# Optimization experiments

Measured on AMD Instinct MI355X. Metric: run time of the kernel, lower is better.

Reference implementation:

```python
import jax, jax.numpy as jnp
import numpy as np

# ---- FNET: small stride-4 CNN feature extractor (3 -> 64 channels) ----

def _conv(x, w, b, stride, pad):
    y = jax.lax.conv_general_dilated(x, w, (stride, stride), [(pad, pad), (pad, pad)],
                                     dimension_numbers=('NCHW', 'OIHW', 'NCHW'))
    return y + b[None, :, None, None]


def _fnet(x, w1, b1, w2, b2, w3, b3):
    x = jax.nn.relu(_conv(x, w1, b1, 2, 3))   # /2
    x = jax.nn.relu(_conv(x, w2, b2, 2, 1))   # /4
    return _conv(x, w3, b3, 1, 1)             # [N, 64, H/4, W/4]


def _bilinear(feat, u, v):
    # feat: [C, Hf, Wf]; u, v: [D, H, W] pixel coords. Zero padding outside.
    C, Hf, Wf = feat.shape
    u0 = jnp.floor(u); v0 = jnp.floor(v)
    du = u - u0; dv = v - v0
    def gather(ui, vi):
        inb = (ui >= 0) & (ui < Wf) & (vi >= 0) & (vi < Hf)
        uic = jnp.clip(ui, 0, Wf - 1).astype(jnp.int32)
        vic = jnp.clip(vi, 0, Hf - 1).astype(jnp.int32)
        return feat[:, vic, uic] * inb[None].astype(feat.dtype)  # [C, D, H, W]
    f00 = gather(u0, v0);     f01 = gather(u0 + 1, v0)
    f10 = gather(u0, v0 + 1); f11 = gather(u0 + 1, v0 + 1)
    return (f00 * ((1 - du) * (1 - dv))[None] + f01 * (du * (1 - dv))[None]
            + f10 * ((1 - du) * dv)[None] + f11 * (du * dv)[None])


def _magnet_f(ref_img, nghbr_imgs, nghbr_poses, is_valid, cam_intrins, d_center,
              w1, b1, w2, b2, w3, b3):
    B = ref_img.shape[0]
    feat_4 = _fnet(jnp.concatenate([ref_img, nghbr_imgs], axis=0), w1, b1, w2, b2, w3, b3)
    ref_feat = feat_4[:B]                      # [B, C, H4, W4]
    ngh_feat = feat_4[B:]                      # [B*V, C, H4, W4]
    BV = ngh_feat.shape[0]; V = BV // B
    C, H4, W4 = ref_feat.shape[1:]
    D = d_center.shape[1]

    R = nghbr_poses[:, :, :3, :3]              # [B, V, 3, 3]
    t = nghbr_poses[:, :, :3, 3]               # [B, V, 3]
    Kinv = jnp.linalg.inv(cam_intrins)         # [B, 3, 3]

    dt = d_center.dtype
    ys, xs = jnp.meshgrid(jnp.arange(H4, dtype=dt), jnp.arange(W4, dtype=dt), indexing='ij')
    pix = jnp.stack([xs, ys, jnp.ones_like(xs)], 0)          # [3, H4, W4]
    rays = jnp.einsum('bij,jhw->bihw', Kinv, pix)            # [B, 3, H4, W4]
    P = d_center[:, None] * rays[:, :, None]                 # [B, 3, D, H4, W4]
    P_src = jnp.einsum('bvij,bjdhw->bvidhw', R, P) + t[..., None, None, None]
    p = jnp.einsum('bij,bvjdhw->bvidhw', cam_intrins, P_src) # [B, V, 3, D, H4, W4]

    z = p[:, :, 2]
    z_ok = z > 1e-3
    zc = jnp.maximum(z, 1e-3)
    u = p[:, :, 0] / zc
    v = p[:, :, 1] / zc                                      # [B, V, D, H4, W4]
    inb = (u >= 0) & (u <= W4 - 1) & (v >= 0) & (v <= H4 - 1)

    warped = jax.vmap(_bilinear)(ngh_feat,
                                 u.reshape(BV, D, H4, W4),
                                 v.reshape(BV, D, H4, W4))   # [B*V, C, D, H4, W4]
    warped = warped.reshape(B, V, C, D, H4, W4)

    cost = jnp.einsum('bchw,bvcdhw->bvdhw', ref_feat, warped) / C  # [B, V, D, H4, W4]
    mask = (is_valid[:, :, None, None, None] & z_ok & inb).astype(cost.dtype)
    cost_volume = (cost * mask).sum(1) / jnp.maximum(mask.sum(1), 1.0)  # [B, D, H4, W4]
    return cost_volume


def setup_inputs() -> dict:
    B, V, H, W, D, C = 2, 4, 480, 640, 5, 64
    H4, W4 = H // 4, W // 4
    ks = jax.random.split(jax.random.key(0), 12)
    ref_img = jax.random.normal(ks[0], (B, 3, H, W), jnp.float32)
    nghbr_imgs = jax.random.normal(ks[1], (B * V, 3, H, W), jnp.float32)
    # near-identity relative poses with small random translations
    poses = jnp.tile(jnp.eye(4, dtype=jnp.float32), (B, V, 1, 1))
    poses = poses.at[:, :, :3, 3].set(0.05 * jax.random.normal(ks[2], (B, V, 3), jnp.float32))
    is_valid = jnp.ones((B, V), dtype=bool)
    K = jnp.array([[144.0, 0.0, 80.0], [0.0, 144.0, 60.0], [0.0, 0.0, 1.0]], jnp.float32)
    cam_intrins = jnp.tile(K, (B, 1, 1))
    d_center = jax.random.uniform(ks[3], (B, D, H4, W4), jnp.float32, 0.5, 5.0)
    w1 = 0.1 * jax.random.normal(ks[4], (32, 3, 7, 7), jnp.float32); b1 = jnp.zeros((32,), jnp.float32)
    w2 = 0.1 * jax.random.normal(ks[5], (C, 32, 3, 3), jnp.float32); b2 = jnp.zeros((C,), jnp.float32)
    w3 = 0.1 * jax.random.normal(ks[6], (C, C, 3, 3), jnp.float32); b3 = jnp.zeros((C,), jnp.float32)
    return {"ref_img": ref_img, "nghbr_imgs": nghbr_imgs, "nghbr_poses": poses,
            "is_valid": is_valid, "cam_intrins": cam_intrins, "d_center": d_center,
            "w1": w1, "b1": b1, "w2": w2, "b2": b2, "w3": w3, "b3": b3}


def reference(ref_img, nghbr_imgs, nghbr_poses, is_valid, cam_intrins, d_center,
              w1, b1, w2, b2, w3, b3):
    return _magnet_f(ref_img, nghbr_imgs, nghbr_poses, is_valid, cam_intrins, d_center,
                     w1, b1, w2, b2, w3, b3)
```

## Files before the change

kernel.cpp:

```cpp
#include <hip/hip_runtime.h>
#include <hip/hip_bf16.h>

#define B_  2
#define V_  4
#define Hin 480
#define Win 640
#define H2  240
#define W2  320
#define H4  120
#define W4  160
#define C1  32
#define C_  64
#define D_  5
#define NIMG 10

#define P1H 242
#define P1W 322
#define P2H 122
#define P2W 162
#define PIH 486
#define PIW 646

typedef __attribute__((ext_vector_type(8))) short short8;
typedef __attribute__((ext_vector_type(4))) float f32x4;

#define OFF_F1HI 0
#define OFF_F1LO 12467840
#define OFF_F2HI 24935680
#define OFF_F2LO 31260160
#define OFF_INHI 24935680
#define OFF_INLO 29645504
#define OFF_F3   0
#define OFF_GEOM 37584640
#define OFF_W1P  37584736
#define OFF_W2P  37590880
#define OFF_W3P  37609312

__global__ void packw_kernel(const float* __restrict__ w, ushort* __restrict__ dst,
                             int CI, int NK, int lo_off) {
    int idx = blockIdx.x * 256 + threadIdx.x;
    int total = 4 * NK * 64 * 8;
    if (idx >= total) return;
    int j = idx & 7;
    int lane = (idx >> 3) & 63;
    int s = (idx >> 9) % NK;
    int t = idx / (NK * 512);
    int k = s * 32 + (lane >> 4) * 8 + j;
    int co = t * 16 + (lane & 15);
    int kyx = k / CI;
    int ci  = k % CI;
    int ky = kyx / 3, kx = kyx % 3;
    float val = w[((co * CI + ci) * 3 + ky) * 3 + kx];
    __hip_bfloat16 h = __float2bfloat16(val);
    float hf = __bfloat162float(h);
    __hip_bfloat16 l = __float2bfloat16(val - hf);
    dst[idx]          = *reinterpret_cast<ushort*>(&h);
    dst[lo_off + idx] = *reinterpret_cast<ushort*>(&l);
}

__global__ void packw1_kernel(const float* __restrict__ w, ushort* __restrict__ dst) {
    int idx = blockIdx.x * 256 + threadIdx.x;
    if (idx >= 6144) return;
    int j = idx & 7;
    int lane = (idx >> 3) & 63;
    int s = (idx >> 9) % 6;
    int t = idx / 3072;
    int g = s * 4 + (lane >> 4);
    int co = t * 16 + (lane & 15);
    float val = 0.0f;
    if (g < 21 && j < 7) {
        int ci = g / 7, ky = g % 7;
        val = w[((co * 3 + ci) * 7 + ky) * 7 + j];
    }
    __hip_bfloat16 h = __float2bfloat16(val);
    float hf = __bfloat162float(h);
    __hip_bfloat16 l = __float2bfloat16(val - hf);
    dst[idx]        = *reinterpret_cast<ushort*>(&h);
    dst[6144 + idx] = *reinterpret_cast<ushort*>(&l);
}

__global__ void packin_kernel(const float* __restrict__ ref, const float* __restrict__ ngh,
                              ushort* __restrict__ ihi, ushort* __restrict__ ilo) {
    int idx = blockIdx.x * 256 + threadIdx.x;
    const int tot = NIMG * 3 * PIH * PIW;
    if (idx >= tot) return;
    int x = idx % PIW;
    int r = idx / PIW;
    int y = r % PIH;
    int rc = r / PIH;
    int ci = rc % 3;
    int n  = rc / 3;
    float val = 0.0f;
    int lx = x - 3, ly = y - 3;
    if (lx >= 0 && lx < Win && ly >= 0 && ly < Hin) {
        const float* img = (n < B_) ? (ref + ((size_t)n * 3 + ci) * Hin * Win)
                                    : (ngh + ((size_t)(n - B_) * 3 + ci) * Hin * Win);
        val = img[(size_t)ly * Win + lx];
    }
    __hip_bfloat16 h = __float2bfloat16(val);
    float hf = __bfloat162float(h);
    __hip_bfloat16 l = __float2bfloat16(val - hf);
    ihi[idx] = *reinterpret_cast<ushort*>(&h);
    ilo[idx] = *reinterpret_cast<ushort*>(&l);
}

__global__ void zerob_kernel(ushort* __restrict__ f1hi, ushort* __restrict__ f1lo,
                             ushort* __restrict__ f2hi, ushort* __restrict__ f2lo) {
    const int F1B = 2 * P1W + 2 * (P1H - 2);
    const int F2B = 2 * P2W + 2 * (P2H - 2);
    const int f1tot = NIMG * F1B * C1;
    const int f2tot = NIMG * F2B * C_;
    int idx = blockIdx.x * 256 + threadIdx.x;
    if (idx < f1tot) {
        int c = idx & 31; int r = idx >> 5;
        int n = r / F1B; int bp = r % F1B;
        int y, x;
        if (bp < P1W)            { y = 0;        x = bp; }
        else if (bp < 2*P1W)     { y = P1H - 1;  x = bp - P1W; }
        else if (bp < 2*P1W + (P1H-2)) { y = bp - 2*P1W + 1;   x = 0; }
        else                     { y = bp - 2*P1W - (P1H-2) + 1; x = P1W - 1; }
        size_t o = (((size_t)n * P1H + y) * P1W + x) * C1 + c;
        f1hi[o] = 0; f1lo[o] = 0;
        return;
    }
    idx -= f1tot;
    if (idx < f2tot) {
        int c = idx & 63; int r = idx >> 6;
        int n = r / F2B; int bp = r % F2B;
        int y, x;
        if (bp < P2W)            { y = 0;        x = bp; }
        else if (bp < 2*P2W)     { y = P2H - 1;  x = bp - P2W; }
        else if (bp < 2*P2W + (P2H-2)) { y = bp - 2*P2W + 1;   x = 0; }
        else                     { y = bp - 2*P2W - (P2H-2) + 1; x = P2W - 1; }
        size_t o = (((size_t)n * P2H + y) * P2W + x) * C_ + c;
        f2hi[o] = 0; f2lo[o] = 0;
    }
}

__global__ void geom_kernel(const float* __restrict__ poses,
                            const float* __restrict__ Kmat,
                            float* __restrict__ geom) {
    int i = threadIdx.x;
    if (i >= B_ * V_) return;
    int b = i / V_;
    const float* Kb = Kmat + b * 9;
    float k00=Kb[0],k01=Kb[1],k02=Kb[2];
    float k10=Kb[3],k11=Kb[4],k12=Kb[5];
    float k20=Kb[6],k21=Kb[7],k22=Kb[8];
    float det = k00*(k11*k22-k12*k21) - k01*(k10*k22-k12*k20) + k02*(k10*k21-k11*k20);
    float id = 1.0f / det;
    float ki[9];
    ki[0]=(k11*k22-k12*k21)*id; ki[1]=(k02*k21-k01*k22)*id; ki[2]=(k01*k12-k02*k11)*id;
    ki[3]=(k12*k20-k10*k22)*id; ki[4]=(k00*k22-k02*k20)*id; ki[5]=(k02*k10-k00*k12)*id;
    ki[6]=(k10*k21-k11*k20)*id; ki[7]=(k01*k20-k00*k21)*id; ki[8]=(k00*k11-k01*k10)*id;
    const float* P = poses + i * 16;
    float R[9] = {P[0],P[1],P[2], P[4],P[5],P[6], P[8],P[9],P[10]};
    float t[3] = {P[3],P[7],P[11]};
    float KR[9];
    for (int r = 0; r < 3; r++)
        for (int c = 0; c < 3; c++)
            KR[r*3+c] = Kb[r*3+0]*R[0*3+c] + Kb[r*3+1]*R[1*3+c] + Kb[r*3+2]*R[2*3+c];
    float* g = geom + i * 12;
    for (int r = 0; r < 3; r++)
        for (int c = 0; c < 3; c++)
            g[r*3+c] = KR[r*3+0]*ki[0*3+c] + KR[r*3+1]*ki[1*3+c] + KR[r*3+2]*ki[2*3+c];
    for (int r = 0; r < 3; r++)
        g[9+r] = Kb[r*3+0]*t[0] + Kb[r*3+1]*t[1] + Kb[r*3+2]*t[2];
}

__global__ __launch_bounds__(256) void conv1_mfma(
        const ushort* __restrict__ ihi, const ushort* __restrict__ ilo,
        const ushort* __restrict__ w1p, const float* __restrict__ b1,
        ushort* __restrict__ f1hi, ushort* __restrict__ f1lo) {
    const int lane = threadIdx.x & 63;
    const int wv   = threadIdx.x >> 6;
    const int n    = blockIdx.y;
    const int px0  = blockIdx.x * 64 + wv * 16;
    const int p    = px0 + (lane & 15);
    const int y = p / W2, x = p % W2;
    const int kg = lane >> 4;
    const ushort* ih = ihi + (size_t)n * 3 * PIH * PIW;
    const ushort* il = ilo + (size_t)n * 3 * PIH * PIW;

    f32x4 acc[2] = {};
#pragma unroll
    for (int s = 0; s < 6; s++) {
        const int g = s * 4 + kg;
        short8 ahi = {}, alo = {};
        if (g < 21) {
            const int ci = g / 7, ky = g % 7;
            const size_t off = ((size_t)(ci * PIH + 2 * y + ky)) * PIW + 2 * x;
            ahi = *reinterpret_cast<const short8*>(ih + off);
            alo = *reinterpret_cast<const short8*>(il + off);
        }
#pragma unroll
        for (int t = 0; t < 2; t++) {
            const int widx = ((t * 6 + s) * 64 + lane) * 8;
            short8 bhi = *reinterpret_cast<const short8*>(w1p + widx);
            short8 blo = *reinterpret_cast<const short8*>(w1p + 6144 + widx);
            acc[t] = __builtin_amdgcn_mfma_f32_16x16x32_bf16(ahi, bhi, acc[t], 0, 0, 0);
            acc[t] = __builtin_amdgcn_mfma_f32_16x16x32_bf16(ahi, blo, acc[t], 0, 0, 0);
            acc[t] = __builtin_amdgcn_mfma_f32_16x16x32_bf16(alo, bhi, acc[t], 0, 0, 0);
        }
    }
#pragma unroll
    for (int t = 0; t < 2; t++) {
        const int co = t * 16 + (lane & 15);
        const float bias = b1[co];
#pragma unroll
        for (int j = 0; j < 4; j++) {
            const int pr = px0 + kg * 4 + j;
            const int oy = pr / W2, ox = pr % W2;
            float val = fmaxf(acc[t][j] + bias, 0.0f);
            __hip_bfloat16 h = __float2bfloat16(val);
            float hf = __bfloat162float(h);
            __hip_bfloat16 l = __float2bfloat16(val - hf);
            const size_t o = (((size_t)n * P1H + (oy + 1)) * P1W + (ox + 1)) * C1 + co;
            f1hi[o] = *reinterpret_cast<ushort*>(&h);
            f1lo[o] = *reinterpret_cast<ushort*>(&l);
        }
    }
}

__global__ __launch_bounds__(256) void conv2_mfma(
        const ushort* __restrict__ f1hi, const ushort* __restrict__ f1lo,
        const ushort* __restrict__ w2p, const float* __restrict__ b2,
        ushort* __restrict__ f2hi, ushort* __restrict__ f2lo) {
    const int lane = threadIdx.x & 63;
    const int wv   = threadIdx.x >> 6;
    const int n    = blockIdx.y;
    const int px0  = blockIdx.x * 64 + wv * 16;
    const int p    = px0 + (lane & 15);
    const int y = p / W4, x = p % W4;
    const int kg = lane >> 4;
    const ushort* ihi = f1hi + (size_t)n * P1H * P1W * C1;
    const ushort* ilo = f1lo + (size_t)n * P1H * P1W * C1;

    f32x4 acc[4] = {};
#pragma unroll
    for (int s = 0; s < 9; s++) {
        const int ky = s / 3, kx = s % 3;
        const int off = ((2 * y + ky) * P1W + (2 * x + kx)) * C1 + kg * 8;
        short8 ahi = *reinterpret_cast<const short8*>(ihi + off);
        short8 alo = *reinterpret_cast<const short8*>(ilo + off);
#pragma unroll
        for (int t = 0; t < 4; t++) {
            const int widx = ((t * 9 + s) * 64 + lane) * 8;
            short8 bhi = *reinterpret_cast<const short8*>(w2p + widx);
            short8 blo = *reinterpret_cast<const short8*>(w2p + 18432 + widx);
            acc[t] = __builtin_amdgcn_mfma_f32_16x16x32_bf16(ahi, bhi, acc[t], 0, 0, 0);
            acc[t] = __builtin_amdgcn_mfma_f32_16x16x32_bf16(ahi, blo, acc[t], 0, 0, 0);
            acc[t] = __builtin_amdgcn_mfma_f32_16x16x32_bf16(alo, bhi, acc[t], 0, 0, 0);
        }
    }
    ushort* ohi = f2hi + (size_t)n * P2H * P2W * C_;
    ushort* olo = f2lo + (size_t)n * P2H * P2W * C_;
#pragma unroll
    for (int t = 0; t < 4; t++) {
        const int co = t * 16 + (lane & 15);
        const float bias = b2[co];
#pragma unroll
        for (int j = 0; j < 4; j++) {
            const int pr = px0 + kg * 4 + j;
            const int yy = pr / W4, xx = pr % W4;
            float val = fmaxf(acc[t][j] + bias, 0.0f);
            __hip_bfloat16 h = __float2bfloat16(val);
            float hf = __bfloat162float(h);
            __hip_bfloat16 l = __float2bfloat16(val - hf);
            const size_t o = (((size_t)(yy + 1)) * P2W + (xx + 1)) * C_ + co;
            ohi[o] = *reinterpret_cast<ushort*>(&h);
            olo[o] = *reinterpret_cast<ushort*>(&l);
        }
    }
}

__global__ __launch_bounds__(256) void conv3_mfma(
        const ushort* __restrict__ f2hi, const ushort* __restrict__ f2lo,
        const ushort* __restrict__ w3p, const float* __restrict__ b3,
        float* __restrict__ f3) {
    const int lane = threadIdx.x & 63;
    const int wv   = threadIdx.x >> 6;
    const int n    = blockIdx.y;
    const int px0  = blockIdx.x * 64 + wv * 16;
    const int p    = px0 + (lane & 15);
    const int y = p / W4, x = p % W4;
    const int kg = lane >> 4;
    const ushort* ihi = f2hi + (size_t)n * P2H * P2W * C_;
    const ushort* ilo = f2lo + (size_t)n * P2H * P2W * C_;

    f32x4 acc[4] = {};
#pragma unroll
    for (int s = 0; s < 18; s++) {
        const int kyx = s >> 1;
        const int ky = kyx / 3, kx = kyx % 3;
        const int ci0 = (s & 1) * 32 + kg * 8;
        const int off = ((y + ky) * P2W + (x + kx)) * C_ + ci0;
        short8 ahi = *reinterpret_cast<const short8*>(ihi + off);
        short8 alo = *reinterpret_cast<const short8*>(ilo + off);
#pragma unroll
        for (int t = 0; t < 4; t++) {
            const int widx = ((t * 18 + s) * 64 + lane) * 8;
            short8 bhi = *reinterpret_cast<const short8*>(w3p + widx);
            short8 blo = *reinterpret_cast<const short8*>(w3p + 36864 + widx);
            acc[t] = __builtin_amdgcn_mfma_f32_16x16x32_bf16(ahi, bhi, acc[t], 0, 0, 0);
            acc[t] = __builtin_amdgcn_mfma_f32_16x16x32_bf16(ahi, blo, acc[t], 0, 0, 0);
            acc[t] = __builtin_amdgcn_mfma_f32_16x16x32_bf16(alo, bhi, acc[t], 0, 0, 0);
        }
    }
    float* op = f3 + (size_t)n * H4 * W4 * C_;
#pragma unroll
    for (int t = 0; t < 4; t++) {
        const int co = t * 16 + (lane & 15);
        const float bias = b3[co];
#pragma unroll
        for (int j = 0; j < 4; j++) {
            const int pr = px0 + kg * 4 + j;
            op[(size_t)pr * C_ + co] = acc[t][j] + bias;
        }
    }
}

__global__ void warpcost_kernel(const float* __restrict__ feat,
                                const float* __restrict__ geom,
                                const float* __restrict__ dc,
                                const int*   __restrict__ valid,
                                float* __restrict__ out) {
    const int wave = threadIdx.x >> 6;
    const int lane = threadIdx.x & 63;
    int pid = blockIdx.x * 4 + wave;
    int b = pid / (H4 * W4);
    int rem = pid % (H4 * W4);
    int h = rem / W4;
    int w = rem % W4;

    const float refc = feat[(((size_t)b * H4 + h) * W4 + w) * C_ + lane];

    float dep[D_];
#pragma unroll
    for (int d = 0; d < D_; d++)
        dep[d] = dc[(((size_t)b * D_ + d) * H4 + h) * W4 + w];

    float accv[D_] = {0.f, 0.f, 0.f, 0.f, 0.f};
    float den[D_]  = {0.f, 0.f, 0.f, 0.f, 0.f};

    for (int v = 0; v < V_; v++) {
        if (!valid[b * V_ + v]) continue;
        const float* g = geom + (b * V_ + v) * 12;
        float rx = g[0] * w + g[1] * h + g[2];
        float ry = g[3] * w + g[4] * h + g[5];
        float rz = g[6] * w + g[7] * h + g[8];
        float c0 = g[9], c1 = g[10], c2 = g[11];
        const float* fimg = feat + (size_t)(B_ + b * V_ + v) * H4 * W4 * C_;
#pragma unroll
        for (int d = 0; d < D_; d++) {
            float px = dep[d] * rx + c0;
            float py = dep[d] * ry + c1;
            float pz = dep[d] * rz + c2;
            bool zok = pz > 0.001f;
            float zc = fmaxf(pz, 0.001f);
            float u  = px / zc;
            float vv = py / zc;
            bool inb = (u >= 0.f) && (u <= (float)(W4 - 1)) &&
                       (vv >= 0.f) && (vv <= (float)(H4 - 1));
            if (zok && inb) {
                float u0f = floorf(u), v0f = floorf(vv);
                float du = u - u0f, dv = vv - v0f;
                int u0 = (int)u0f, v0 = (int)v0f;
                int u1 = min(u0 + 1, W4 - 1), v1 = min(v0 + 1, H4 - 1);
                const float* r00 = fimg + ((size_t)v0 * W4 + u0) * C_;
                const float* r01 = fimg + ((size_t)v0 * W4 + u1) * C_;
                const float* r10 = fimg + ((size_t)v1 * W4 + u0) * C_;
                const float* r11 = fimg + ((size_t)v1 * W4 + u1) * C_;
                float f00 = r00[lane], f01 = r01[lane];
                float f10 = r10[lane], f11 = r11[lane];
                float wa = (1.f - du) * (1.f - dv);
                float wb = du * (1.f - dv);
                float wc = (1.f - du) * dv;
                float wd = du * dv;
                accv[d] += f00 * wa + f01 * wb + f10 * wc + f11 * wd;
                den[d]  += 1.f;
            }
        }
    }

#pragma unroll
    for (int d = 0; d < D_; d++) {
        float s = refc * accv[d];
        for (int off = 32; off > 0; off >>= 1) s += __shfl_xor(s, off, 64);
        if (lane == 0) {
            out[(((size_t)b * D_ + d) * H4 + h) * W4 + w] =
                (s * (1.0f / (float)C_)) / fmaxf(den[d], 1.0f);
        }
    }
}

extern "C" void kernel_launch(void* const* d_in, const int* in_sizes, int n_in,
                              void* d_out, int out_size, void* d_ws, size_t ws_size,
                              hipStream_t stream) {
    const float* ref_img  = (const float*)d_in[0];
    const float* ngh_img  = (const float*)d_in[1];
    const float* poses    = (const float*)d_in[2];
    const int*   is_valid = (const int*)  d_in[3];
    const float* K        = (const float*)d_in[4];
    const float* dc       = (const float*)d_in[5];
    const float* w1 = (const float*)d_in[6];
    const float* b1 = (const float*)d_in[7];
    const float* w2 = (const float*)d_in[8];
    const float* b2 = (const float*)d_in[9];
    const float* w3 = (const float*)d_in[10];
    const float* b3 = (const float*)d_in[11];
    float* out = (float*)d_out;

    float* ws = (float*)d_ws;
    ushort* f1hi = (ushort*)(ws + OFF_F1HI);
    ushort* f1lo = (ushort*)(ws + OFF_F1LO);
    ushort* f2hi = (ushort*)(ws + OFF_F2HI);
    ushort* f2lo = (ushort*)(ws + OFF_F2LO);
    ushort* inhi = (ushort*)(ws + OFF_INHI);
    ushort* inlo = (ushort*)(ws + OFF_INLO);
    float*  f3   = ws + OFF_F3;
    float*  geom = ws + OFF_GEOM;
    ushort* w1p  = (ushort*)(ws + OFF_W1P);
    ushort* w2p  = (ushort*)(ws + OFF_W2P);
    ushort* w3p  = (ushort*)(ws + OFF_W3P);

    geom_kernel<<<1, 64, 0, stream>>>(poses, K, geom);
    packw1_kernel<<<24, 256, 0, stream>>>(w1, w1p);
    packw_kernel<<<(4*9*64*8 + 255)/256, 256, 0, stream>>>(w2, w2p, C1, 9, 18432);
    packw_kernel<<<(4*18*64*8 + 255)/256, 256, 0, stream>>>(w3, w3p, C_, 18, 36864);
    packin_kernel<<<(NIMG*3*PIH*PIW + 255)/256, 256, 0, stream>>>(ref_img, ngh_img, inhi, inlo);

    conv1_mfma<<<dim3(H2*W2/64, NIMG), 256, 0, stream>>>(inhi, inlo, w1p, b1, f1hi, f1lo);
    {
        const int ztot = NIMG*(2*P1W + 2*(P1H-2))*C1 + NIMG*(2*P2W + 2*(P2H-2))*C_;
        zerob_kernel<<<(ztot + 255)/256, 256, 0, stream>>>(f1hi, f1lo, f2hi, f2lo);
    }
    conv2_mfma<<<dim3(H4*W4/64, NIMG), 256, 0, stream>>>(f1hi, f1lo, w2p, b2, f2hi, f2lo);
    conv3_mfma<<<dim3(H4*W4/64, NIMG), 256, 0, stream>>>(f2hi, f2lo, w3p, b3, f3);

    warpcost_kernel<<<(B_*H4*W4)/4, 256, 0, stream>>>(f3, geom, dc, is_valid, out);
}
```

Baseline: 453.6 us.

## Precompute bilinear sample offsets and weights in a separate kernel before warpcost

Adds a samp_kernel that computes, once per (b, v, d, pixel), the projected bilinear corner offsets, the four weights and a validity bit, and stores them in a workspace region that is free by the time it runs. The warpcost kernel then loads these records and does unconditional, branch-free gathers. This removes the projection math, the divides and the divergent branches that every lane of a 64-lane wave repeated for the same pixel. In exchange it adds one kernel launch and extra global traffic to write and read the precomputed records. Masked samples now do real loads with zero weights instead of being skipped.

New measurement: 438.0 us. -3.4%, faster.

```diff
diff --git a/kernel.cpp b/kernel.cpp
--- a/kernel.cpp
+++ b/kernel.cpp
@@ -13,6 +13,7 @@
 #define C_  64
 #define D_  5
 #define NIMG 10
+#define HW4 (H4*W4)
 
 #define P1H 242
 #define P1W 322
@@ -31,6 +32,8 @@
 #define OFF_INHI 24935680
 #define OFF_INLO 29645504
 #define OFF_F3   0
+#define OFF_SAMPW 12467840
+#define OFF_SAMPM 15539840
 #define OFF_GEOM 37584640
 #define OFF_W1P  37584736
 #define OFF_W2P  37590880
@@ -320,66 +323,78 @@
     }
 }
 
-__global__ void warpcost_kernel(const float* __restrict__ feat,
-                                const float* __restrict__ geom,
-                                const float* __restrict__ dc,
-                                const int*   __restrict__ valid,
-                                float* __restrict__ out) {
+__global__ void samp_kernel(const float* __restrict__ geom,
+                            const float* __restrict__ dc,
+                            const int*   __restrict__ valid,
+                            f32x4* __restrict__ sw, int* __restrict__ sm) {
+    int idx = blockIdx.x * 256 + threadIdx.x;
+    if (idx >= B_ * V_ * D_ * HW4) return;
+    int hw = idx % HW4;
+    int r  = idx / HW4;
+    int d = r % D_;  r /= D_;
+    int v = r % V_;  int b = r / V_;
+    int h = hw / W4, w = hw % W4;
+
+    float dep = dc[((size_t)(b * D_ + d)) * HW4 + hw];
+    const float* g = geom + (b * V_ + v) * 12;
+    float px = dep * (g[0] * w + g[1] * h + g[2]) + g[9];
+    float py = dep * (g[3] * w + g[4] * h + g[5]) + g[10];
+    float pz = dep * (g[6] * w + g[7] * h + g[8]) + g[11];
+    bool zok = pz > 0.001f;
+    float zc = fmaxf(pz, 0.001f);
+    float u  = px / zc;
+    float vv = py / zc;
+    bool inb = (u >= 0.f) && (u <= (float)(W4 - 1)) &&
+               (vv >= 0.f) && (vv <= (float)(H4 - 1));
+    bool m = zok && inb && (valid[b * V_ + v] != 0);
+
+    f32x4 wgt = {0.f, 0.f, 0.f, 0.f};
+    int rec = 0;
+    if (m) {
+        float u0f = floorf(u), v0f = floorf(vv);
+        float du = u - u0f, dv = vv - v0f;
+        int u0 = (int)u0f, v0 = (int)v0f;
+        int off00 = v0 * W4 + u0;
+        int off10 = min(v0 + 1, H4 - 1) * W4 + u0;
+        wgt[0] = (1.f - du) * (1.f - dv);
+        wgt[1] = du * (1.f - dv);
+        wgt[2] = (1.f - du) * dv;
+        wgt[3] = du * dv;
+        rec = off00 | (off10 << 15) | (1 << 30);
+    }
+    sw[idx] = wgt;
+    sm[idx] = rec;
+}
+
+__global__ __launch_bounds__(256) void warpcost_kernel(
+        const float* __restrict__ feat,
+        const f32x4* __restrict__ sw, const int* __restrict__ sm,
+        float* __restrict__ out) {
     const int wave = threadIdx.x >> 6;
     const int lane = threadIdx.x & 63;
     int pid = blockIdx.x * 4 + wave;
-    int b = pid / (H4 * W4);
-    int rem = pid % (H4 * W4);
-    int h = rem / W4;
-    int w = rem % W4;
-
-    const float refc = feat[(((size_t)b * H4 + h) * W4 + w) * C_ + lane];
-
-    float dep[D_];
-#pragma unroll
-    for (int d = 0; d < D_; d++)
-        dep[d] = dc[(((size_t)b * D_ + d) * H4 + h) * W4 + w];
+    int b = pid / HW4;
+    int hw = pid % HW4;
+
+    const float refc = feat[((size_t)b * HW4 + hw) * C_ + lane];
 
     float accv[D_] = {0.f, 0.f, 0.f, 0.f, 0.f};
     float den[D_]  = {0.f, 0.f, 0.f, 0.f, 0.f};
 
+#pragma unroll
     for (int v = 0; v < V_; v++) {
-        if (!valid[b * V_ + v]) continue;
-        const float* g = geom + (b * V_ + v) * 12;
-        float rx = g[0] * w + g[1] * h + g[2];
-        float ry = g[3] * w + g[4] * h + g[5];
-        float rz = g[6] * w + g[7] * h + g[8];
-        float c0 = g[9], c1 = g[10], c2 = g[11];
-        const float* fimg = feat + (size_t)(B_ + b * V_ + v) * H4 * W4 * C_;
+        const float* fimg = feat + (size_t)(B_ + b * V_ + v) * HW4 * C_;
+        const int rbase = ((b * V_ + v) * D_) * HW4 + hw;
 #pragma unroll
         for (int d = 0; d < D_; d++) {
-            float px = dep[d] * rx + c0;
-            float py = dep[d] * ry + c1;
-            float pz = dep[d] * rz + c2;
-            bool zok = pz > 0.001f;
-            float zc = fmaxf(pz, 0.001f);
-            float u  = px / zc;
-            float vv = py / zc;
-            bool inb = (u >= 0.f) && (u <= (float)(W4 - 1)) &&
-                       (vv >= 0.f) && (vv <= (float)(H4 - 1));
-            if (zok && inb) {
-                float u0f = floorf(u), v0f = floorf(vv);
-                float du = u - u0f, dv = vv - v0f;
-                int u0 = (int)u0f, v0 = (int)v0f;
-                int u1 = min(u0 + 1, W4 - 1), v1 = min(v0 + 1, H4 - 1);
-                const float* r00 = fimg + ((size_t)v0 * W4 + u0) * C_;
-                const float* r01 = fimg + ((size_t)v0 * W4 + u1) * C_;
-                const float* r10 = fimg + ((size_t)v1 * W4 + u0) * C_;
-                const float* r11 = fimg + ((size_t)v1 * W4 + u1) * C_;
-                float f00 = r00[lane], f01 = r01[lane];
-                float f10 = r10[lane], f11 = r11[lane];
-                float wa = (1.f - du) * (1.f - dv);
-                float wb = du * (1.f - dv);
-                float wc = (1.f - du) * dv;
-                float wd = du * dv;
-                accv[d] += f00 * wa + f01 * wb + f10 * wc + f11 * wd;
-                den[d]  += 1.f;
-            }
+            int rec  = sm[rbase + d * HW4];
+            f32x4 wv = sw[rbase + d * HW4];
+            int off00 = rec & 0x7FFF;
+            int off10 = (rec >> 15) & 0x7FFF;
+            const float* p0 = fimg + (size_t)off00 * C_ + lane;
+            const float* p1 = fimg + (size_t)off10 * C_ + lane;
+            accv[d] += p0[0] * wv[0] + p0[C_] * wv[1] + p1[0] * wv[2] + p1[C_] * wv[3];
+            den[d]  += (float)((rec >> 30) & 1);
         }
     }
 
@@ -388,7 +403,7 @@
         float s = refc * accv[d];
         for (int off = 32; off > 0; off >>= 1) s += __shfl_xor(s, off, 64);
         if (lane == 0) {
-            out[(((size_t)b * D_ + d) * H4 + h) * W4 + w] =
+            out[((size_t)b * D_ + d) * HW4 + hw] =
                 (s * (1.0f / (float)C_)) / fmaxf(den[d], 1.0f);
         }
     }
@@ -419,6 +434,8 @@
     ushort* inhi = (ushort*)(ws + OFF_INHI);
     ushort* inlo = (ushort*)(ws + OFF_INLO);
     float*  f3   = ws + OFF_F3;
+    f32x4*  sw   = (f32x4*)(ws + OFF_SAMPW);
+    int*    sm   = (int*)  (ws + OFF_SAMPM);
     float*  geom = ws + OFF_GEOM;
     ushort* w1p  = (ushort*)(ws + OFF_W1P);
     ushort* w2p  = (ushort*)(ws + OFF_W2P);
@@ -436,7 +453,8 @@
         zerob_kernel<<<(ztot + 255)/256, 256, 0, stream>>>(f1hi, f1lo, f2hi, f2lo);
     }
     conv2_mfma<<<dim3(H4*W4/64, NIMG), 256, 0, stream>>>(f1hi, f1lo, w2p, b2, f2hi, f2lo);
+    samp_kernel<<<(B_*V_*D_*HW4 + 255)/256, 256, 0, stream>>>(geom, dc, is_valid, sw, sm);
     conv3_mfma<<<dim3(H4*W4/64, NIMG), 256, 0, stream>>>(f2hi, f2lo, w3p, b3, f3);
 
-    warpcost_kernel<<<(B_*H4*W4)/4, 256, 0, stream>>>(f3, geom, dc, is_valid, out);
-}
+    warpcost_kernel<<<(B_*HW4)/4, 256, 0, stream>>>(f3, sw, sm, out);
+}
```
